# Kernel tuning notes

Measured on AMD Instinct MI355X. Metric: run time of the kernel, lower is better.

Reference implementation:

```python
import jax, jax.numpy as jnp
import numpy as np

N = 50000      # nodes
E = 1600000    # edges (avg degree 32)
D_IN = 128
HID = 64


def setup_inputs() -> dict:
    key = jax.random.key(0)
    ks = jax.random.split(key, 7)
    x = jax.random.normal(ks[0], (N, D_IN), dtype=jnp.float32)
    ei = jax.random.randint(ks[1], (2, E), 0, N, dtype=jnp.int32)
    ew = jax.random.uniform(ks[2], (E,), dtype=jnp.float32)
    # GCNConv linear weights (glorot-ish scale); lin has no bias, conv bias added post-aggregation
    W1 = jax.random.normal(ks[3], (HID, D_IN), dtype=jnp.float32) * (1.0 / np.sqrt(D_IN))
    b1 = jnp.zeros((HID,), dtype=jnp.float32)
    W2 = jax.random.normal(ks[4], (HID, HID), dtype=jnp.float32) * (1.0 / np.sqrt(HID))
    b2 = jnp.zeros((HID,), dtype=jnp.float32)
    return {"x": x, "ei": ei, "ew": ew, "W1": W1, "b1": b1, "W2": W2, "b2": b2}


def _gcn_conv(x, src, dst, ew_all, W, b, n_nodes):
    """PyG GCNConv: gcn_norm (self-loops already appended) + x@W.T, gather-scale-scatter, +b."""
    deg = jax.ops.segment_sum(ew_all, dst, num_segments=n_nodes)  # dst-side weighted degree
    dinv = jnp.where(deg > 0, jax.lax.rsqrt(deg), 0.0)            # deg^{-1/2}, inf->0
    norm = dinv[src] * ew_all * dinv[dst]                          # [E+N]
    h = x @ W.T                                                    # [N, hid]
    msg = h[src] * norm[:, None]                                   # gather + scale
    out = jax.ops.segment_sum(msg, dst, num_segments=n_nodes)     # scatter-add
    return out + b


def reference(x, ei, ew, W1, b1, W2, b2):
    n_nodes = x.shape[0]
    # add self loops once (fill value 1.0), shared by both conv layers
    loop = jnp.arange(n_nodes, dtype=ei.dtype)
    src = jnp.concatenate([ei[0], loop])
    dst = jnp.concatenate([ei[1], loop])
    ew_all = jnp.concatenate([ew, jnp.ones((n_nodes,), dtype=ew.dtype)])

    h1 = jax.nn.relu(_gcn_conv(x, src, dst, ew_all, W1, b1, n_nodes))
    # dropout is identity in eval mode
    h2 = _gcn_conv(h1, src, dst, ew_all, W2, b2, n_nodes)
    return h2 + h1
```

## Files before the change

### kernel.cpp

```cpp
#include <hip/hip_runtime.h>

#define HID 64
#define DIN 128
#define NBLK 512
#define CSH 14
#define CAP (1 << CSH)
#define PAD 68

typedef unsigned long long ull;
typedef unsigned short u16;

static __device__ __forceinline__ u16 f2bf(float f) {
  unsigned u = __float_as_uint(f);
  unsigned lsb = (u >> 16) & 1u;
  u += 0x7fffu + lsb;
  return (u16)(u >> 16);
}


template <int K, int NT, bool XT_PRELOADED>
__device__ __forceinline__ void gemm_tile(const float* __restrict__ X,
                                          const float* __restrict__ W,
                                          u16* __restrict__ out,
                                          float* XT, float* WL,
                                          int n0, int n_nodes, int tid) {
  constexpr int ROWS = NT / 8;
  const int tx = tid & 15;
  const int ty = tid >> 4;
  float acc[2][4] = {{0.f}};

  for (int ph = 0; ph < K / 64; ++ph) {
    const int d0 = ph * 64;
    __syncthreads();
    if (!XT_PRELOADED) {
#pragma unroll
      for (int k = 0; k < 2; ++k) {
        int f = tid + k * NT;
        int r = f >> 4, q = f & 15;
        int n = n0 + r;
        float4 xv = (n < n_nodes)
          ? *reinterpret_cast<const float4*>(&X[(size_t)n * K + d0 + 4 * q])
          : make_float4(0.f, 0.f, 0.f, 0.f);
        *reinterpret_cast<float4*>(&XT[r * PAD + 4 * q]) = xv;
      }
    }
#pragma unroll
    for (int k = 0; k < 1024 / NT; ++k) {
      int gq = tid + k * NT;
      int qd = gq >> 6, j = gq & 63;
      float4 wv = *reinterpret_cast<const float4*>(&W[(size_t)j * K + d0 + 4 * qd]);
      WL[(4 * qd + 0) * PAD + j] = wv.x;
      WL[(4 * qd + 1) * PAD + j] = wv.y;
      WL[(4 * qd + 2) * PAD + j] = wv.z;
      WL[(4 * qd + 3) * PAD + j] = wv.w;
    }
    __syncthreads();
#pragma unroll 4
    for (int dd = 0; dd < 64; dd += 4) {
      float4 ws[4];
#pragma unroll
      for (int dk = 0; dk < 4; ++dk)
        ws[dk] = *reinterpret_cast<const float4*>(&WL[(dd + dk) * PAD + 4 * tx]);
      float4 x0 = *reinterpret_cast<const float4*>(&XT[ty * PAD + dd]);
      float4 x1 = *reinterpret_cast<const float4*>(&XT[(ty + ROWS / 2) * PAD + dd]);
      float xm0[4] = {x0.x, x0.y, x0.z, x0.w};
      float xm1[4] = {x1.x, x1.y, x1.z, x1.w};
#pragma unroll
      for (int dk = 0; dk < 4; ++dk) {
        acc[0][0] = fmaf(xm0[dk], ws[dk].x, acc[0][0]);
        acc[0][1] = fmaf(xm0[dk], ws[dk].y, acc[0][1]);
        acc[0][2] = fmaf(xm0[dk], ws[dk].z, acc[0][2]);
        acc[0][3] = fmaf(xm0[dk], ws[dk].w, acc[0][3]);
        acc[1][0] = fmaf(xm1[dk], ws[dk].x, acc[1][0]);
        acc[1][1] = fmaf(xm1[dk], ws[dk].y, acc[1][1]);
        acc[1][2] = fmaf(xm1[dk], ws[dk].z, acc[1][2]);
        acc[1][3] = fmaf(xm1[dk], ws[dk].w, acc[1][3]);
      }
    }
  }

#pragma unroll
  for (int mi = 0; mi < 2; ++mi) {
    int n = n0 + mi * (ROWS / 2) + ty;
    if (n < n_nodes) {
      ushort4 o = make_ushort4(f2bf(acc[mi][0]), f2bf(acc[mi][1]),
                               f2bf(acc[mi][2]), f2bf(acc[mi][3]));
      *reinterpret_cast<ushort4*>(&out[(size_t)n * HID + 4 * tx]) = o;
    }
  }
}


__global__ __launch_bounds__(512) void k_build_gemm(const int* __restrict__ src,
                                                    const int* __restrict__ dst,
                                                    const float* __restrict__ ew,
                                                    int* __restrict__ cursor,
                                                    int2* __restrict__ bufA,
                                                    int E, int chunk,
                                                    const float* __restrict__ x,
                                                    const float* __restrict__ W1,
                                                    u16* __restrict__ h,
                                                    int n_nodes) {
  __shared__ float S[9216];
  int b = blockIdx.x, tid = threadIdx.x;
  if (b >= NBLK) {
    gemm_tile<DIN, 512, false>(x, W1, h, S, S + 64 * PAD, (b - NBLK) * 64, n_nodes, tid);
    return;
  }
  int2* lbuf  = (int2*)S;
  int*  lhist = (int*)&S[8192];
  int*  lstart= (int*)&S[8448];
  int*  lcur  = (int*)&S[8704];
  int*  gofs  = (int*)&S[8960];
  if (tid < 256) lhist[tid] = 0;
  __syncthreads();
  int e0 = b * chunk, e1 = min(E, e0 + chunk);
  int m = e1 - e0;
  int4 s4[2], d4[2];
  float4 w4[2];
  bool val[2];
#pragma unroll
  for (int it = 0; it < 2; ++it) {
    int e = e0 + 4 * (tid + it * 512);
    val[it] = (e < e1) && (e < e0 + 4096);
    if (val[it]) {
      s4[it] = *reinterpret_cast<const int4*>(&src[e]);
      d4[it] = *reinterpret_cast<const int4*>(&dst[e]);
      w4[it] = *reinterpret_cast<const float4*>(&ew[e]);
      atomicAdd(&lhist[d4[it].x >> 8], 1);
      atomicAdd(&lhist[d4[it].y >> 8], 1);
      atomicAdd(&lhist[d4[it].z >> 8], 1);
      atomicAdd(&lhist[d4[it].w >> 8], 1);
    }
  }
  __syncthreads();
  int own = (tid < 256) ? lhist[tid] : 0;
  for (int o = 1; o < 256; o <<= 1) {
    int u = 0;
    if (tid < 256 && tid >= o) u = lhist[tid - o];
    __syncthreads();
    if (tid < 256) lhist[tid] += u;
    __syncthreads();
  }
  if (tid < 256) {
    int excl = lhist[tid] - own;
    lstart[tid] = excl;
    lcur[tid] = excl;
    int g = (own > 0) ? atomicAdd(&cursor[tid], own) : 0;
    gofs[tid] = (tid << CSH) + g - excl;
  }
  __syncthreads();
#pragma unroll
  for (int it = 0; it < 2; ++it) {
    if (val[it]) {
      int p0 = atomicAdd(&lcur[d4[it].x >> 8], 1);
      lbuf[p0] = make_int2(__float_as_int(w4[it].x),
                           (int)(((unsigned)s4[it].x << 16) | (unsigned)d4[it].x));
      int p1 = atomicAdd(&lcur[d4[it].y >> 8], 1);
      lbuf[p1] = make_int2(__float_as_int(w4[it].y),
                           (int)(((unsigned)s4[it].y << 16) | (unsigned)d4[it].y));
      int p2 = atomicAdd(&lcur[d4[it].z >> 8], 1);
      lbuf[p2] = make_int2(__float_as_int(w4[it].z),
                           (int)(((unsigned)s4[it].z << 16) | (unsigned)d4[it].z));
      int p3 = atomicAdd(&lcur[d4[it].w >> 8], 1);
      lbuf[p3] = make_int2(__float_as_int(w4[it].w),
                           (int)(((unsigned)s4[it].w << 16) | (unsigned)d4[it].w));
    }
  }
  __syncthreads();
  int mc = min(m, 4096);
  for (int j = tid; j < mc; j += 512) {
    int2 r = lbuf[j];
    int bkt = (int)(((unsigned)r.y & 0xffffu) >> 8);
    bufA[gofs[bkt] + j] = r;
  }
  for (int e = e0 + 4096 + tid; e < e1; e += 512) {
    int s = src[e], d = dst[e];
    int g = atomicAdd(&cursor[d >> 8], 1);
    bufA[((d >> 8) << CSH) + g] = make_int2(__float_as_int(ew[e]),
                                            (int)(((unsigned)s << 16) | (unsigned)d));
  }
}


__global__ __launch_bounds__(1024) void k_passB(const int2* __restrict__ bufA,
                                                const int* __restrict__ cursor,
                                                int2* __restrict__ bufB,
                                                int* __restrict__ offs,
                                                int* __restrict__ cnt,
                                                float* __restrict__ dinv,
                                                int NBC, int N) {
  __shared__ int2 sbuf[4096];
  __shared__ int h2[256];
  __shared__ int exf[256];
  __shared__ int wr[256];
  __shared__ int cst[257];
  __shared__ int ccur[256];
  __shared__ float dg[256];
  int bin = blockIdx.x, tid = threadIdx.x;
  int bbase = bin << CSH;
  int m = cursor[bin];
  if (tid < 256) { h2[tid] = 0; dg[tid] = 0.f; wr[tid] = 0; }
  __syncthreads();
  int2 rloc[16];
#pragma unroll
  for (int k = 0; k < 16; ++k) {
    int i = tid + k * 1024;
    if (i < m) {
      rloc[k] = bufA[bbase + i];
      int fb = (int)((unsigned)rloc[k].y & 255u);
      atomicAdd(&h2[fb], 1);
      atomicAdd(&dg[fb], __int_as_float(rloc[k].x));
    }
  }
  __syncthreads();
  int own = (tid < 256) ? h2[tid] : 0;
  for (int o = 1; o < 256; o <<= 1) {
    int u = 0;
    if (tid < 256 && tid >= o) u = h2[tid - o];
    __syncthreads();
    if (tid < 256) h2[tid] += u;
    __syncthreads();
  }
  int nd = (bin << 8) + tid;
  if (tid < 256) {
    int excl = h2[tid] - own;
    exf[tid] = excl;
    if (nd < N) {
      offs[nd] = bbase + excl;
      cnt[nd] = own;
      dinv[nd] = rsqrtf(1.0f + dg[tid]);
    }
  }
  __syncthreads();
  for (int c = 0; c < 4; ++c) {
    int mm = m - c * 4096;
    mm = (mm < 0) ? 0 : ((mm > 4096) ? 4096 : mm);
    if (tid < 256) ccur[tid] = 0;
    __syncthreads();
    if (mm > 0) {
#pragma unroll
      for (int kk = 0; kk < 4; ++kk) {
        int k = 4 * c + kk;
        int i = tid + k * 1024;
        if (i < m) atomicAdd(&ccur[(unsigned)rloc[k].y & 255u], 1);
      }
    }
    __syncthreads();
    if (tid < 64) {
      int l = tid;
      int b0 = ccur[4 * l], b1 = ccur[4 * l + 1],
          b2 = ccur[4 * l + 2], b3 = ccur[4 * l + 3];
      int tot = b0 + b1 + b2 + b3;
      int inc = tot;
      for (int o = 1; o < 64; o <<= 1) {
        int u = __shfl_up(inc, o, 64);
        if (l >= o) inc += u;
      }
      int pre = inc - tot;
      cst[4 * l] = pre;
      cst[4 * l + 1] = pre + b0;
      cst[4 * l + 2] = pre + b0 + b1;
      cst[4 * l + 3] = pre + b0 + b1 + b2;
      if (l == 63) cst[256] = inc;
    }
    __syncthreads();
    if (tid < 256) ccur[tid] = cst[tid];
    __syncthreads();
    if (mm > 0) {
#pragma unroll
      for (int kk = 0; kk < 4; ++kk) {
        int k = 4 * c + kk;
        int i = tid + k * 1024;
        if (i < m) {
          int fb = (int)((unsigned)rloc[k].y & 255u);
          int p = atomicAdd(&ccur[fb], 1);
          sbuf[p] = rloc[k];
        }
      }
    }
    __syncthreads();
    for (int j = tid; j < mm; j += 1024) {
      int2 r = sbuf[j];
      unsigned sd = (unsigned)r.y;
      int fb = (int)(sd & 255u);
      int slot = bbase + exf[fb] + wr[fb] + (j - cst[fb]);
      bufB[slot] = make_int2(r.x, (int)(sd >> 16));
    }
    __syncthreads();
    if (tid < 256) wr[tid] += cst[tid + 1] - cst[tid];
    __syncthreads();
  }
}


__device__ __forceinline__ void bfma8(const uint4& v, float w, float* a) {
  a[0] = fmaf(__uint_as_float(v.x << 16), w, a[0]);
  a[1] = fmaf(__uint_as_float(v.x & 0xffff0000u), w, a[1]);
  a[2] = fmaf(__uint_as_float(v.y << 16), w, a[2]);
  a[3] = fmaf(__uint_as_float(v.y & 0xffff0000u), w, a[3]);
  a[4] = fmaf(__uint_as_float(v.z << 16), w, a[4]);
  a[5] = fmaf(__uint_as_float(v.z & 0xffff0000u), w, a[5]);
  a[6] = fmaf(__uint_as_float(v.w << 16), w, a[6]);
  a[7] = fmaf(__uint_as_float(v.w & 0xffff0000u), w, a[7]);
}

__device__ __forceinline__ void agg_node(const u16* __restrict__ h,
                                         const int2* __restrict__ recs,
                                         const float* __restrict__ dinv,
                                         int beg, int end, int node, float di,
                                         int lane, int p8, float* r) {
  float a[8], b[8];
  {
    uint4 v = *reinterpret_cast<const uint4*>(&h[(size_t)node * HID + p8]);
    a[0] = __uint_as_float(v.x << 16) * di;
    a[1] = __uint_as_float(v.x & 0xffff0000u) * di;
    a[2] = __uint_as_float(v.y << 16) * di;
    a[3] = __uint_as_float(v.y & 0xffff0000u) * di;
    a[4] = __uint_as_float(v.z << 16) * di;
    a[5] = __uint_as_float(v.z & 0xffff0000u) * di;
    a[6] = __uint_as_float(v.w << 16) * di;
    a[7] = __uint_as_float(v.w & 0xffff0000u) * di;
#pragma unroll
    for (int j = 0; j < 8; ++j) b[j] = 0.f;
  }

  const int gb = lane & 56;
  const int l7 = lane & 7;
  int i = beg;
  if (i + 8 <= end) {
    ull rr = *reinterpret_cast<const ull*>(&recs[i + l7]);
    float dv = dinv[(int)(rr >> 32)];
    for (;;) {
      float wd = __uint_as_float((unsigned)rr) * dv;
      ull ru = (rr & 0xffffffff00000000ull) | (ull)__float_as_uint(wd);
      bool more = (i + 16 <= end);
      ull rr_n = 0; float dv_n = 0.f;
      if (more) {
        rr_n = *reinterpret_cast<const ull*>(&recs[i + 8 + l7]);
        dv_n = dinv[(int)(rr_n >> 32)];
      }
#pragma unroll
      for (int k = 0; k < 8; ++k) {
        ull q = __shfl(ru, gb | k, 64);
        float wk = __uint_as_float((unsigned)q);
        int sk = (int)(q >> 32);
        uint4 vk = *reinterpret_cast<const uint4*>(&h[(size_t)sk * HID + p8]);
        bfma8(vk, wk, (k & 1) ? b : a);
      }
      i += 8;
      if (!more) break;
      rr = rr_n; dv = dv_n;
    }
  }
  if (i + 4 <= end) {
    int2 r0 = recs[i];     int2 r1 = recs[i + 1];
    int2 r2 = recs[i + 2]; int2 r3 = recs[i + 3];
    uint4 v0 = *reinterpret_cast<const uint4*>(&h[(size_t)r0.y * HID + p8]);
    uint4 v1 = *reinterpret_cast<const uint4*>(&h[(size_t)r1.y * HID + p8]);
    uint4 v2 = *reinterpret_cast<const uint4*>(&h[(size_t)r2.y * HID + p8]);
    uint4 v3 = *reinterpret_cast<const uint4*>(&h[(size_t)r3.y * HID + p8]);
    bfma8(v0, __int_as_float(r0.x) * dinv[r0.y], a);
    bfma8(v1, __int_as_float(r1.x) * dinv[r1.y], b);
    bfma8(v2, __int_as_float(r2.x) * dinv[r2.y], a);
    bfma8(v3, __int_as_float(r3.x) * dinv[r3.y], b);
    i += 4;
  }
  if (i + 2 <= end) {
    int2 r0 = recs[i];     int2 r1 = recs[i + 1];
    uint4 v0 = *reinterpret_cast<const uint4*>(&h[(size_t)r0.y * HID + p8]);
    uint4 v1 = *reinterpret_cast<const uint4*>(&h[(size_t)r1.y * HID + p8]);
    bfma8(v0, __int_as_float(r0.x) * dinv[r0.y], a);
    bfma8(v1, __int_as_float(r1.x) * dinv[r1.y], b);
    i += 2;
  }
  if (i < end) {
    int2 r0 = recs[i];
    uint4 v0 = *reinterpret_cast<const uint4*>(&h[(size_t)r0.y * HID + p8]);
    bfma8(v0, __int_as_float(r0.x) * dinv[r0.y], a);
  }
#pragma unroll
  for (int j = 0; j < 8; ++j) r[j] = (a[j] + b[j]) * di;
}


__global__ __launch_bounds__(256) void k_agg_gemm(const u16* __restrict__ h,
                                                  const int2* __restrict__ recs,
                                                  const int* __restrict__ offs,
                                                  const int* __restrict__ cnt,
                                                  const float* __restrict__ dinv,
                                                  const float* __restrict__ bias,
                                                  const float* __restrict__ W2,
                                                  float* __restrict__ h1,
                                                  u16* __restrict__ h2,
                                                  int n_nodes) {
  __shared__ float S[(32 + 64) * PAD];
  float* XT = S;
  float* WL = S + 32 * PAD;
  int tid = threadIdx.x;
  int lane = tid & 63;
  int p8 = (lane & 7) * 8;
  int nl = (tid >> 6) * 8 + (lane >> 3);
  int node = blockIdx.x * 32 + nl;
  if (node < n_nodes) {
    float di = dinv[node];
    float r[8];
    agg_node(h, recs, dinv, offs[node], offs[node] + cnt[node], node, di,
             lane, p8, r);
    float4 bb0 = *reinterpret_cast<const float4*>(&bias[p8]);
    float4 bb1 = *reinterpret_cast<const float4*>(&bias[p8 + 4]);
    r[0] += bb0.x; r[1] += bb0.y; r[2] += bb0.z; r[3] += bb0.w;
    r[4] += bb1.x; r[5] += bb1.y; r[6] += bb1.z; r[7] += bb1.w;
#pragma unroll
    for (int j = 0; j < 8; ++j) r[j] = fmaxf(r[j], 0.f);
    float4 lo = make_float4(r[0], r[1], r[2], r[3]);
    float4 hi = make_float4(r[4], r[5], r[6], r[7]);
    *reinterpret_cast<float4*>(&h1[(size_t)node * HID + p8]) = lo;
    *reinterpret_cast<float4*>(&h1[(size_t)node * HID + p8 + 4]) = hi;
    *reinterpret_cast<float4*>(&XT[nl * PAD + p8]) = lo;
    *reinterpret_cast<float4*>(&XT[nl * PAD + p8 + 4]) = hi;
  }
  gemm_tile<HID, 256, true>(nullptr, W2, h2, XT, WL, blockIdx.x * 32, n_nodes, tid);
}


__global__ __launch_bounds__(256) void k_agg2(const u16* __restrict__ h,
                                              const int2* __restrict__ recs,
                                              const int* __restrict__ offs,
                                              const int* __restrict__ cnt,
                                              const float* __restrict__ dinv,
                                              const float* __restrict__ bias,
                                              const float* __restrict__ resid,
                                              float* __restrict__ out, int n_nodes) {
  int tid = threadIdx.x;
  int lane = tid & 63;
  int p8 = (lane & 7) * 8;
  int node = (blockIdx.x * 4 + (tid >> 6)) * 8 + (lane >> 3);
  if (node >= n_nodes) return;
  float di = dinv[node];
  float r[8];
  agg_node(h, recs, dinv, offs[node], offs[node] + cnt[node], node, di,
           lane, p8, r);
  float4 bb0 = *reinterpret_cast<const float4*>(&bias[p8]);
  float4 bb1 = *reinterpret_cast<const float4*>(&bias[p8 + 4]);
  float4 rs0 = *reinterpret_cast<const float4*>(&resid[(size_t)node * HID + p8]);
  float4 rs1 = *reinterpret_cast<const float4*>(&resid[(size_t)node * HID + p8 + 4]);
  r[0] += bb0.x + rs0.x; r[1] += bb0.y + rs0.y;
  r[2] += bb0.z + rs0.z; r[3] += bb0.w + rs0.w;
  r[4] += bb1.x + rs1.x; r[5] += bb1.y + rs1.y;
  r[6] += bb1.z + rs1.z; r[7] += bb1.w + rs1.w;
  *reinterpret_cast<float4*>(&out[(size_t)node * HID + p8]) =
      make_float4(r[0], r[1], r[2], r[3]);
  *reinterpret_cast<float4*>(&out[(size_t)node * HID + p8 + 4]) =
      make_float4(r[4], r[5], r[6], r[7]);
}


extern "C" void kernel_launch(void* const* d_in, const int* in_sizes, int n_in,
                              void* d_out, int out_size, void* d_ws, size_t ws_size,
                              hipStream_t stream) {
  const float* x  = (const float*)d_in[0];
  const int*   ei = (const int*)d_in[1];
  const float* ew = (const float*)d_in[2];
  const float* W1 = (const float*)d_in[3];
  const float* b1 = (const float*)d_in[4];
  const float* W2 = (const float*)d_in[5];
  const float* b2 = (const float*)d_in[6];
  float* out = (float*)d_out;

  const int N = in_sizes[0] / DIN;
  const int E = in_sizes[2];
  const int* src = ei;
  const int* dst = ei + E;

  const int NBC = (N + 255) >> 8;
  const int chunk = (((E + NBLK - 1) / NBLK) + 3) & ~3;
  const int nslab = NBC << CSH;

  char* p = (char*)d_ws;
  auto carve = [&](size_t bytes) {
    char* r = p;
    p += (bytes + 255) & ~(size_t)255;
    return r;
  };
  int*   cursor = (int*)carve(256 * 4);
  int*   offs   = (int*)carve((size_t)N * 4);
  int*   cnt    = (int*)carve((size_t)N * 4);
  float* dinv   = (float*)carve((size_t)N * 4);
  int2*  bufA   = (int2*)carve((size_t)nslab * 8);
  int2*  bufB   = (int2*)carve((size_t)nslab * 8);
  u16*   h      = (u16*)carve((size_t)N * HID * 2);
  u16*   h2     = (u16*)carve((size_t)N * HID * 2);
  float* h1     = (float*)carve((size_t)N * HID * 4);

  int gblk  = (N + 63) / 64;
  int gblk2 = (N + 31) / 32;
  int ablk  = (N + 31) / 32;

  hipMemsetAsync(cursor, 0, 256 * 4, stream);
  k_build_gemm<<<NBLK + gblk, 512, 0, stream>>>(src, dst, ew, cursor, bufA, E, chunk,
                                                x, W1, h, N);
  k_passB<<<NBC, 1024, 0, stream>>>(bufA, cursor, bufB, offs, cnt, dinv, NBC, N);
  k_agg_gemm<<<gblk2, 256, 0, stream>>>(h, bufB, offs, cnt, dinv, b1, W2, h1, h2, N);
  k_agg2<<<ablk, 256, 0, stream>>>(h2, bufB, offs, cnt, dinv, b2, h1, out, N);
}
```

Before: 212.4 us.

## Simplify bucket scatter to direct atomics and pretranspose W2 for agg-gemm

The second bucketing pass drops its chunked LDS counting sort and writes each record straight to its per-node slot via a shared-memory atomic cursor. Degree accumulation moves into that scatter loop. W2 is transposed once by an extra block in the first kernel, so the fused aggregate+GEMM kernel reads weights from global/L2 instead of staging them in LDS with an extra barrier. This cuts LDS use and barriers, but edge order within each node becomes nondeterministic, so the float summation order varies between runs.

```diff
diff --git a/kernel.cpp b/kernel.cpp
--- a/kernel.cpp
+++ b/kernel.cpp
@@ -18,13 +18,12 @@
 }
 
 
-template <int K, int NT, bool XT_PRELOADED>
+template <int K>
 __device__ __forceinline__ void gemm_tile(const float* __restrict__ X,
                                           const float* __restrict__ W,
                                           u16* __restrict__ out,
                                           float* XT, float* WL,
                                           int n0, int n_nodes, int tid) {
-  constexpr int ROWS = NT / 8;
   const int tx = tid & 15;
   const int ty = tid >> 4;
   float acc[2][4] = {{0.f}};
@@ -32,21 +31,19 @@
   for (int ph = 0; ph < K / 64; ++ph) {
     const int d0 = ph * 64;
     __syncthreads();
-    if (!XT_PRELOADED) {
-#pragma unroll
-      for (int k = 0; k < 2; ++k) {
-        int f = tid + k * NT;
-        int r = f >> 4, q = f & 15;
-        int n = n0 + r;
-        float4 xv = (n < n_nodes)
-          ? *reinterpret_cast<const float4*>(&X[(size_t)n * K + d0 + 4 * q])
-          : make_float4(0.f, 0.f, 0.f, 0.f);
-        *reinterpret_cast<float4*>(&XT[r * PAD + 4 * q]) = xv;
-      }
-    }
-#pragma unroll
-    for (int k = 0; k < 1024 / NT; ++k) {
-      int gq = tid + k * NT;
+#pragma unroll
+    for (int k = 0; k < 2; ++k) {
+      int f = tid + k * 512;
+      int r = f >> 4, q = f & 15;
+      int n = n0 + r;
+      float4 xv = (n < n_nodes)
+        ? *reinterpret_cast<const float4*>(&X[(size_t)n * K + d0 + 4 * q])
+        : make_float4(0.f, 0.f, 0.f, 0.f);
+      *reinterpret_cast<float4*>(&XT[r * PAD + 4 * q]) = xv;
+    }
+#pragma unroll
+    for (int k = 0; k < 2; ++k) {
+      int gq = tid + k * 512;
       int qd = gq >> 6, j = gq & 63;
       float4 wv = *reinterpret_cast<const float4*>(&W[(size_t)j * K + d0 + 4 * qd]);
       WL[(4 * qd + 0) * PAD + j] = wv.x;
@@ -62,7 +59,7 @@
       for (int dk = 0; dk < 4; ++dk)
         ws[dk] = *reinterpret_cast<const float4*>(&WL[(dd + dk) * PAD + 4 * tx]);
       float4 x0 = *reinterpret_cast<const float4*>(&XT[ty * PAD + dd]);
-      float4 x1 = *reinterpret_cast<const float4*>(&XT[(ty + ROWS / 2) * PAD + dd]);
+      float4 x1 = *reinterpret_cast<const float4*>(&XT[(ty + 32) * PAD + dd]);
       float xm0[4] = {x0.x, x0.y, x0.z, x0.w};
       float xm1[4] = {x1.x, x1.y, x1.z, x1.w};
 #pragma unroll
@@ -81,7 +78,7 @@
 
 #pragma unroll
   for (int mi = 0; mi < 2; ++mi) {
-    int n = n0 + mi * (ROWS / 2) + ty;
+    int n = n0 + mi * 32 + ty;
     if (n < n_nodes) {
       ushort4 o = make_ushort4(f2bf(acc[mi][0]), f2bf(acc[mi][1]),
                                f2bf(acc[mi][2]), f2bf(acc[mi][3]));
@@ -100,11 +97,21 @@
                                                     const float* __restrict__ x,
                                                     const float* __restrict__ W1,
                                                     u16* __restrict__ h,
-                                                    int n_nodes) {
+                                                    int n_nodes,
+                                                    const float* __restrict__ W2,
+                                                    float* __restrict__ WT2,
+                                                    int ntile) {
   __shared__ float S[9216];
   int b = blockIdx.x, tid = threadIdx.x;
+  if (b >= NBLK + ntile) {
+    for (int i = tid; i < HID * HID; i += 512) {
+      int d = i >> 6, j = i & 63;
+      WT2[i] = W2[j * HID + d];
+    }
+    return;
+  }
   if (b >= NBLK) {
-    gemm_tile<DIN, 512, false>(x, W1, h, S, S + 64 * PAD, (b - NBLK) * 64, n_nodes, tid);
+    gemm_tile<DIN>(x, W1, h, S, S + 64 * PAD, (b - NBLK) * 64, n_nodes, tid);
     return;
   }
   int2* lbuf  = (int2*)S;
@@ -190,17 +197,13 @@
                                                 int* __restrict__ cnt,
                                                 float* __restrict__ dinv,
                                                 int NBC, int N) {
-  __shared__ int2 sbuf[4096];
+  int bin = blockIdx.x, tid = threadIdx.x;
   __shared__ int h2[256];
-  __shared__ int exf[256];
-  __shared__ int wr[256];
-  __shared__ int cst[257];
-  __shared__ int ccur[256];
+  __shared__ int cur[256];
   __shared__ float dg[256];
-  int bin = blockIdx.x, tid = threadIdx.x;
   int bbase = bin << CSH;
   int m = cursor[bin];
-  if (tid < 256) { h2[tid] = 0; dg[tid] = 0.f; wr[tid] = 0; }
+  if (tid < 256) { h2[tid] = 0; dg[tid] = 0.f; }
   __syncthreads();
   int2 rloc[16];
 #pragma unroll
@@ -208,9 +211,7 @@
     int i = tid + k * 1024;
     if (i < m) {
       rloc[k] = bufA[bbase + i];
-      int fb = (int)((unsigned)rloc[k].y & 255u);
-      atomicAdd(&h2[fb], 1);
-      atomicAdd(&dg[fb], __int_as_float(rloc[k].x));
+      atomicAdd(&h2[(unsigned)rloc[k].y & 255u], 1);
     }
   }
   __syncthreads();
@@ -225,72 +226,24 @@
   int nd = (bin << 8) + tid;
   if (tid < 256) {
     int excl = h2[tid] - own;
-    exf[tid] = excl;
-    if (nd < N) {
-      offs[nd] = bbase + excl;
-      cnt[nd] = own;
-      dinv[nd] = rsqrtf(1.0f + dg[tid]);
-    }
-  }
-  __syncthreads();
-  for (int c = 0; c < 4; ++c) {
-    int mm = m - c * 4096;
-    mm = (mm < 0) ? 0 : ((mm > 4096) ? 4096 : mm);
-    if (tid < 256) ccur[tid] = 0;
-    __syncthreads();
-    if (mm > 0) {
-#pragma unroll
-      for (int kk = 0; kk < 4; ++kk) {
-        int k = 4 * c + kk;
-        int i = tid + k * 1024;
-        if (i < m) atomicAdd(&ccur[(unsigned)rloc[k].y & 255u], 1);
-      }
-    }
-    __syncthreads();
-    if (tid < 64) {
-      int l = tid;
-      int b0 = ccur[4 * l], b1 = ccur[4 * l + 1],
-          b2 = ccur[4 * l + 2], b3 = ccur[4 * l + 3];
-      int tot = b0 + b1 + b2 + b3;
-      int inc = tot;
-      for (int o = 1; o < 64; o <<= 1) {
-        int u = __shfl_up(inc, o, 64);
-        if (l >= o) inc += u;
-      }
-      int pre = inc - tot;
-      cst[4 * l] = pre;
-      cst[4 * l + 1] = pre + b0;
-      cst[4 * l + 2] = pre + b0 + b1;
-      cst[4 * l + 3] = pre + b0 + b1 + b2;
-      if (l == 63) cst[256] = inc;
-    }
-    __syncthreads();
-    if (tid < 256) ccur[tid] = cst[tid];
-    __syncthreads();
-    if (mm > 0) {
-#pragma unroll
-      for (int kk = 0; kk < 4; ++kk) {
-        int k = 4 * c + kk;
-        int i = tid + k * 1024;
-        if (i < m) {
-          int fb = (int)((unsigned)rloc[k].y & 255u);
-          int p = atomicAdd(&ccur[fb], 1);
-          sbuf[p] = rloc[k];
-        }
-      }
-    }
-    __syncthreads();
-    for (int j = tid; j < mm; j += 1024) {
-      int2 r = sbuf[j];
+    cur[tid] = excl;
+    if (nd < N) { offs[nd] = bbase + excl; cnt[nd] = own; }
+  }
+  __syncthreads();
+#pragma unroll
+  for (int k = 0; k < 16; ++k) {
+    int i = tid + k * 1024;
+    if (i < m) {
+      int2 r = rloc[k];
       unsigned sd = (unsigned)r.y;
-      int fb = (int)(sd & 255u);
-      int slot = bbase + exf[fb] + wr[fb] + (j - cst[fb]);
-      bufB[slot] = make_int2(r.x, (int)(sd >> 16));
-    }
-    __syncthreads();
-    if (tid < 256) wr[tid] += cst[tid + 1] - cst[tid];
-    __syncthreads();
-  }
+      int dl = (int)(sd & 255u);
+      int p = atomicAdd(&cur[dl], 1);
+      bufB[bbase + p] = make_int2(r.x, (int)(sd >> 16));
+      atomicAdd(&dg[dl], __int_as_float(r.x));
+    }
+  }
+  __syncthreads();
+  if (tid < 256 && nd < N) dinv[nd] = rsqrtf(1.0f + dg[tid]);
 }
 
 
@@ -390,18 +343,17 @@
                                                   const int* __restrict__ cnt,
                                                   const float* __restrict__ dinv,
                                                   const float* __restrict__ bias,
-                                                  const float* __restrict__ W2,
+                                                  const float* __restrict__ WT2,
                                                   float* __restrict__ h1,
                                                   u16* __restrict__ h2,
                                                   int n_nodes) {
-  __shared__ float S[(32 + 64) * PAD];
-  float* XT = S;
-  float* WL = S + 32 * PAD;
+  __shared__ float XT[32 * PAD];
   int tid = threadIdx.x;
   int lane = tid & 63;
   int p8 = (lane & 7) * 8;
   int nl = (tid >> 6) * 8 + (lane >> 3);
-  int node = blockIdx.x * 32 + nl;
+  int n0 = blockIdx.x * 32;
+  int node = n0 + nl;
   if (node < n_nodes) {
     float di = dinv[node];
     float r[8];
@@ -420,7 +372,41 @@
     *reinterpret_cast<float4*>(&XT[nl * PAD + p8]) = lo;
     *reinterpret_cast<float4*>(&XT[nl * PAD + p8 + 4]) = hi;
   }
-  gemm_tile<HID, 256, true>(nullptr, W2, h2, XT, WL, blockIdx.x * 32, n_nodes, tid);
+  __syncthreads();
+  const int tx = tid & 15;
+  const int ty = tid >> 4;
+  float acc[2][4] = {{0.f}};
+#pragma unroll 4
+  for (int dd = 0; dd < 64; dd += 4) {
+    float4 ws[4];
+#pragma unroll
+    for (int dk = 0; dk < 4; ++dk)
+      ws[dk] = *reinterpret_cast<const float4*>(&WT2[(dd + dk) * 64 + 4 * tx]);
+    float4 x0 = *reinterpret_cast<const float4*>(&XT[ty * PAD + dd]);
+    float4 x1 = *reinterpret_cast<const float4*>(&XT[(ty + 16) * PAD + dd]);
+    float xm0[4] = {x0.x, x0.y, x0.z, x0.w};
+    float xm1[4] = {x1.x, x1.y, x1.z, x1.w};
+#pragma unroll
+    for (int dk = 0; dk < 4; ++dk) {
+      acc[0][0] = fmaf(xm0[dk], ws[dk].x, acc[0][0]);
+      acc[0][1] = fmaf(xm0[dk], ws[dk].y, acc[0][1]);
+      acc[0][2] = fmaf(xm0[dk], ws[dk].z, acc[0][2]);
+      acc[0][3] = fmaf(xm0[dk], ws[dk].w, acc[0][3]);
+      acc[1][0] = fmaf(xm1[dk], ws[dk].x, acc[1][0]);
+      acc[1][1] = fmaf(xm1[dk], ws[dk].y, acc[1][1]);
+      acc[1][2] = fmaf(xm1[dk], ws[dk].z, acc[1][2]);
+      acc[1][3] = fmaf(xm1[dk], ws[dk].w, acc[1][3]);
+    }
+  }
+#pragma unroll
+  for (int mi = 0; mi < 2; ++mi) {
+    int n = n0 + mi * 16 + ty;
+    if (n < n_nodes) {
+      ushort4 o = make_ushort4(f2bf(acc[mi][0]), f2bf(acc[mi][1]),
+                               f2bf(acc[mi][2]), f2bf(acc[mi][3]));
+      *reinterpret_cast<ushort4*>(&h2[(size_t)n * HID + 4 * tx]) = o;
+    }
+  }
 }
 
 
@@ -492,15 +478,16 @@
   u16*   h      = (u16*)carve((size_t)N * HID * 2);
   u16*   h2     = (u16*)carve((size_t)N * HID * 2);
   float* h1     = (float*)carve((size_t)N * HID * 4);
+  float* WT2    = (float*)carve((size_t)HID * HID * 4);
 
   int gblk  = (N + 63) / 64;
   int gblk2 = (N + 31) / 32;
   int ablk  = (N + 31) / 32;
 
   hipMemsetAsync(cursor, 0, 256 * 4, stream);
-  k_build_gemm<<<NBLK + gblk, 512, 0, stream>>>(src, dst, ew, cursor, bufA, E, chunk,
-                                                x, W1, h, N);
+  k_build_gemm<<<NBLK + gblk + 1, 512, 0, stream>>>(src, dst, ew, cursor, bufA, E,
+                                                    chunk, x, W1, h, N, W2, WT2, gblk);
   k_passB<<<NBC, 1024, 0, stream>>>(bufA, cursor, bufB, offs, cnt, dinv, NBC, N);
-  k_agg_gemm<<<gblk2, 256, 0, stream>>>(h, bufB, offs, cnt, dinv, b1, W2, h1, h2, N);
+  k_agg_gemm<<<gblk2, 256, 0, stream>>>(h, bufB, offs, cnt, dinv, b1, WT2, h1, h2, N);
   k_agg2<<<ablk, 256, 0, stream>>>(h2, bufB, offs, cnt, dinv, b2, h1, out, N);
 }
```

Measured after the change: 214.8 us. About the same (+1.1%).
